# Kernel tuning notes

Measured on AMD Instinct MI355X. Metric: run time of the kernel, lower is better.

## Reference

```python
import jax, jax.numpy as jnp
import numpy as np

B, S, D, H = 2, 2048, 1024, 16
DK = D // H

def setup_inputs() -> dict:
    key = jax.random.key(0)
    ks = jax.random.split(key, 12)
    def lin(k, shape, fan_in):
        bound = 1.0 / np.sqrt(fan_in)
        return jax.random.uniform(k, shape, jnp.float32, -bound, bound)
    inp = {
        'Q': jax.random.normal(ks[0], (B, S, D), jnp.float32),
        'K': jax.random.normal(ks[1], (B, S, D), jnp.float32),
        'V': jax.random.normal(ks[2], (B, S, D), jnp.float32),
        # padding mask: last 128 key positions of batch element 0 are padding
        'padding_mask': jnp.ones((B, 1, 1, S), jnp.int32).at[0, :, :, -128:].set(0),
        # causal look-ahead mask
        'look_ahead_mask': jnp.tril(jnp.ones((S, S), jnp.int32))[None, None],
        'Wq': lin(ks[3], (D, D), D), 'bq': lin(ks[4], (D,), D),
        'Wk': lin(ks[5], (D, D), D), 'bk': lin(ks[6], (D,), D),
        'Wv': lin(ks[7], (D, D), D), 'bv': lin(ks[8], (D,), D),
        'Wo': lin(ks[9], (D, D), D), 'bo': lin(ks[10], (D,), D),
    }
    return inp

def _split_heads(x):
    # [B,S,D] -> [B,H,S,DK]
    b, s, _ = x.shape
    return x.reshape(b, s, H, DK).transpose(0, 2, 1, 3)

def reference(Q, K, V, padding_mask, look_ahead_mask, Wq, bq, Wk, bk, Wv, bv, Wo, bo):
    q = _split_heads(Q @ Wq.T + bq)  # [B,H,S,DK]
    k = _split_heads(K @ Wk.T + bk)
    v = _split_heads(V @ Wv.T + bv)
    scores = jnp.einsum('bhqd,bhkd->bhqk', q, k) / np.sqrt(DK).astype(np.float32)
    neg_inf = jnp.float32(-jnp.inf)
    scores = jnp.where(padding_mask == 0, neg_inf, scores)
    scores = jnp.where(look_ahead_mask == 0, neg_inf, scores)
    weights = jax.nn.softmax(scores, axis=-1)  # dropout is identity in eval mode
    x = jnp.einsum('bhqk,bhkd->bhqd', weights, v)  # [B,H,S,DK]
    x = x.transpose(0, 2, 1, 3).reshape(Q.shape[0], Q.shape[1], D)
    return x @ Wo.T + bo
```

## Files before the change

### kernel.cpp

```cpp
#include <hip/hip_runtime.h>
#include <hip/hip_bf16.h>

#define B_   2
#define S_   2048
#define D_   1024
#define H_   16
#define DK_  64

typedef unsigned short u16;
typedef __attribute__((ext_vector_type(8))) short bf16x8;
typedef __attribute__((ext_vector_type(4))) float f32x4;

#define CHUNK_   12
#define NSLOT_   48

static __device__ __forceinline__ u16 f2bf(float f) {
  union { float f; unsigned u; } v; v.f = f;
  unsigned r = v.u + 0x7FFF + ((v.u >> 16) & 1);
  return (u16)(r >> 16);
}

static __device__ __forceinline__ void gl_lds16(const void* g, void* l) {
  __builtin_amdgcn_global_load_lds(
      (const __attribute__((address_space(1))) void*)g,
      (__attribute__((address_space(3))) void*)l, 16, 0, 0);
}

__global__ void cvt7(const float4* __restrict__ i0, const float4* __restrict__ i1,
                     const float4* __restrict__ i2, const float4* __restrict__ i3,
                     const float4* __restrict__ i4, const float4* __restrict__ i5,
                     const float4* __restrict__ i6,
                     ushort4* __restrict__ o0, ushort4* __restrict__ o1,
                     ushort4* __restrict__ o2, ushort4* __restrict__ o3,
                     ushort4* __restrict__ o4, ushort4* __restrict__ o5,
                     ushort4* __restrict__ o6, int nbig, int nsmall) {
  int y = blockIdx.y;
  const float4* in; ushort4* out; int bound;
  switch (y) {
    case 0: in = i0; out = o0; bound = nbig; break;
    case 1: in = i1; out = o1; bound = nbig; break;
    case 2: in = i2; out = o2; bound = nbig; break;
    case 3: in = i3; out = o3; bound = nsmall; break;
    case 4: in = i4; out = o4; bound = nsmall; break;
    case 5: in = i5; out = o5; bound = nsmall; break;
    default: in = i6; out = o6; bound = nsmall; break;
  }
  int i = blockIdx.x * blockDim.x + threadIdx.x;
  if (i < bound) {
    float4 v = in[i];
    ushort4 r;
    r.x = f2bf(v.x); r.y = f2bf(v.y); r.z = f2bf(v.z); r.w = f2bf(v.w);
    out[i] = r;
  }
}

__launch_bounds__(256, 2)
__global__ void gemm_qkv(const u16* __restrict__ Xq, const u16* __restrict__ Xk, const u16* __restrict__ Xv,
                         const u16* __restrict__ Wq, const u16* __restrict__ Wk, const u16* __restrict__ Wv,
                         const float* __restrict__ bq, const float* __restrict__ bk, const float* __restrict__ bv,
                         u16* __restrict__ outq, u16* __restrict__ outk, u16* __restrict__ outv) {
  const int z = blockIdx.z;
  const u16* Am; const u16* Bm; int m0, n0;
  if (z == 2) { Am = Wv; Bm = Xv; m0 = blockIdx.x * 128; n0 = blockIdx.y * 128; }
  else if (z == 1) { Am = Xk; Bm = Wk; m0 = blockIdx.y * 128; n0 = blockIdx.x * 128; }
  else { Am = Xq; Bm = Wq; m0 = blockIdx.y * 128; n0 = blockIdx.x * 128; }
  const float* bias = (z == 0) ? bq : (z == 1) ? bk : bv;

  __shared__ __align__(16) u16 As[128 * 32];
  __shared__ __align__(16) u16 Bs[128 * 32];

  const int tid = threadIdx.x, lane = tid & 63, w = tid >> 6;
  const int q = lane >> 4, cl = lane & 15;
  const int wr = w >> 1, wc = w & 1;

  f32x4 acc[4][4] = {};

  for (int k0 = 0; k0 < D_; k0 += 32) {
#pragma unroll
    for (int i = 0; i < 2; ++i) {
      int cb = (i * 4 + w) * 64;
      int ch = cb + lane;
      int row = ch >> 2, ko = (ch & 3) << 3;
      gl_lds16(Am + (size_t)(m0 + row) * D_ + k0 + ko, As + cb * 8);
      gl_lds16(Bm + (size_t)(n0 + row) * D_ + k0 + ko, Bs + cb * 8);
    }
    __syncthreads();

    bf16x8 af[4], bfr[4];
#pragma unroll
    for (int r = 0; r < 4; ++r) af[r]  = *(const bf16x8*)(As + (wr * 64 + r * 16 + cl) * 32 + q * 8);
#pragma unroll
    for (int c = 0; c < 4; ++c) bfr[c] = *(const bf16x8*)(Bs + (wc * 64 + c * 16 + cl) * 32 + q * 8);
#pragma unroll
    for (int r = 0; r < 4; ++r)
#pragma unroll
      for (int c = 0; c < 4; ++c)
        acc[r][c] = __builtin_amdgcn_mfma_f32_16x16x32_bf16(af[r], bfr[c], acc[r][c], 0, 0, 0);
    __syncthreads();
  }

  if (z == 2) {
#pragma unroll
    for (int r = 0; r < 4; ++r) {
#pragma unroll
      for (int rr = 0; rr < 4; ++rr) {
        int j = m0 + wr * 64 + r * 16 + q * 4 + rr;
        float bval = bias[j];
        int hh = j >> 6, dk = j & 63;
#pragma unroll
        for (int c = 0; c < 4; ++c) {
          int n = n0 + wc * 64 + c * 16 + cl;
          int bb = n >> 11, s = n & (S_ - 1);
          outv[((size_t)(bb * H_ + hh) * DK_ + dk) * S_ + s] = f2bf(acc[r][c][rr] + bval);
        }
      }
    }
  } else {
    const float scale = (z == 0) ? 0.125f : 1.0f;
    u16* o = (z == 0) ? outq : outk;
#pragma unroll
    for (int c = 0; c < 4; ++c) {
      int j = n0 + wc * 64 + c * 16 + cl;
      float bval = bias[j];
      int hh = j >> 6, dk = j & 63;
#pragma unroll
      for (int r = 0; r < 4; ++r) {
#pragma unroll
        for (int rr = 0; rr < 4; ++rr) {
          int n = m0 + wr * 64 + r * 16 + q * 4 + rr;
          int bb = n >> 11, s = n & (S_ - 1);
          o[((size_t)(bb * H_ + hh) * S_ + s) * DK_ + dk] = f2bf((acc[r][c][rr] + bval) * scale);
        }
      }
    }
  }
}

__launch_bounds__(256, 4)
__global__ void attn(const u16* __restrict__ qh, const u16* __restrict__ kh,
                     const u16* __restrict__ vt, const int* __restrict__ pad,
                     u16* __restrict__ attn_out, float* __restrict__ Po, float* __restrict__ Pl) {
  __shared__ __align__(16) u16 Ks[64 * 64];
  __shared__ __align__(16) u16 Vs[64 * 64];
  __shared__ __align__(16) u16 Ps[4][16 * 72];
  __shared__ float Kbias[64];

  const int tid = threadIdx.x, lane = tid & 63, w = tid >> 6;
  const int q = lane >> 4, cl = lane & 15;
  const int h = blockIdx.y, b = blockIdx.z;

  const int x = blockIdx.x;
  int qt, ch, nch;
  if (x < 24)      { qt = 24 + x / 3;          ch = x % 3;       nch = 3; }
  else if (x < 48) { int y = x - 24; qt = 12 + y / 2; ch = y & 1; nch = 2; }
  else             { qt = x - 48;              ch = 0;           nch = 1; }
  const int qb = qt * 64;
  const int t0 = ch * CHUNK_;
  const int t1 = (qt < t0 + CHUNK_ - 1) ? qt : (t0 + CHUNK_ - 1);

  const u16* Q = qh + (size_t)(b * H_ + h) * S_ * DK_;
  const u16* K = kh + (size_t)(b * H_ + h) * S_ * DK_;
  const u16* V = vt + (size_t)(b * H_ + h) * DK_ * S_;
  const int* pm = pad + b * S_;

  const int qr0 = qb + w * 16;
  bf16x8 qf0 = *(const bf16x8*)(Q + (qr0 + cl) * DK_ + q * 8);
  bf16x8 qf1 = *(const bf16x8*)(Q + (qr0 + cl) * DK_ + 32 + q * 8);

  f32x4 o[4] = {};
  float ls[4] = {0.f, 0.f, 0.f, 0.f};
  u16* Pw = Ps[w];

  for (int it = t0; it <= t1; ++it) {
    const int kb = it << 6;
#pragma unroll
    for (int i = 0; i < 2; ++i) {
      int s = (i * 4 + w) * 64 + lane;
      int row = s >> 3;
      int c = (s & 7) ^ (row & 7);
      gl_lds16(K + (size_t)(kb + row) * DK_ + (c << 3), Ks + (size_t)s * 8);
      gl_lds16(V + (size_t)row * S_ + kb + (c << 3), Vs + (size_t)s * 8);
    }
    if (tid < 64) {
      Kbias[tid] = (pm[kb + tid] != 0) ? -6.0f : -3e38f;
    }
    __syncthreads();

    f32x4 sa[4];
#pragma unroll
    for (int ct = 0; ct < 4; ++ct) {
      int rk = ct * 16 + cl;
      int c0 = q ^ (rk & 7);
      bf16x8 kf0 = *(const bf16x8*)(Ks + rk * 64 + (c0 << 3));
      bf16x8 kf1 = *(const bf16x8*)(Ks + rk * 64 + ((c0 ^ 4) << 3));
      f32x4 zz = {};
      zz = __builtin_amdgcn_mfma_f32_16x16x32_bf16(qf0, kf0, zz, 0, 0, 0);
      zz = __builtin_amdgcn_mfma_f32_16x16x32_bf16(qf1, kf1, zz, 0, 0, 0);
      sa[ct] = zz;
    }

    if (it < qt) {
#pragma unroll
      for (int ct = 0; ct < 4; ++ct) {
        float kbv = Kbias[ct * 16 + cl];
#pragma unroll
        for (int rr = 0; rr < 4; ++rr) {
          float p = __expf(sa[ct][rr] + kbv);
          ls[rr] += p;
          Pw[(q * 4 + rr) * 72 + ct * 16 + cl] = f2bf(p);
        }
      }
    } else {
#pragma unroll
      for (int ct = 0; ct < 4; ++ct) {
        int kg = kb + ct * 16 + cl;
        float kbv = Kbias[ct * 16 + cl];
#pragma unroll
        for (int rr = 0; rr < 4; ++rr) {
          int qg = qr0 + q * 4 + rr;
          float p = (kg <= qg) ? __expf(sa[ct][rr] + kbv) : 0.f;
          ls[rr] += p;
          Pw[(q * 4 + rr) * 72 + ct * 16 + cl] = f2bf(p);
        }
      }
    }

    bf16x8 pf0 = *(const bf16x8*)(Pw + cl * 72 + q * 8);
    bf16x8 pf1 = *(const bf16x8*)(Pw + cl * 72 + 32 + q * 8);

#pragma unroll
    for (int ct = 0; ct < 4; ++ct) {
      int rv = ct * 16 + cl;
      int c0 = q ^ (rv & 7);
      bf16x8 vf0 = *(const bf16x8*)(Vs + rv * 64 + (c0 << 3));
      bf16x8 vf1 = *(const bf16x8*)(Vs + rv * 64 + ((c0 ^ 4) << 3));
      o[ct] = __builtin_amdgcn_mfma_f32_16x16x32_bf16(pf0, vf0, o[ct], 0, 0, 0);
      o[ct] = __builtin_amdgcn_mfma_f32_16x16x32_bf16(pf1, vf1, o[ct], 0, 0, 0);
    }
    __syncthreads();
  }

  if (nch == 1) {
#pragma unroll
    for (int rr = 0; rr < 4; ++rr) {
      float l = ls[rr];
      l += __shfl_xor(l, 1, 64);
      l += __shfl_xor(l, 2, 64);
      l += __shfl_xor(l, 4, 64);
      l += __shfl_xor(l, 8, 64);
      float inv = 1.0f / l;
      int qg = qr0 + q * 4 + rr;
      size_t base = (size_t)(b * S_ + qg) * D_ + h * DK_;
#pragma unroll
      for (int ct = 0; ct < 4; ++ct)
        attn_out[base + ct * 16 + cl] = f2bf(o[ct][rr] * inv);
    }
  } else {
    int pq = qt - 12;
    int off = (pq < 12) ? pq * 2 : 24 + (pq - 12) * 3;
    size_t slot = (size_t)(b * H_ + h) * NSLOT_ + off + ch;
#pragma unroll
    for (int rr = 0; rr < 4; ++rr) {
      float l = ls[rr];
      l += __shfl_xor(l, 1, 64);
      l += __shfl_xor(l, 2, 64);
      l += __shfl_xor(l, 4, 64);
      l += __shfl_xor(l, 8, 64);
      int rl = w * 16 + q * 4 + rr;
      if (cl == 0) Pl[slot * 64 + rl] = l;
      float* po = Po + ((size_t)slot * 64 + rl) * 64;
#pragma unroll
      for (int ct = 0; ct < 4; ++ct)
        po[ct * 16 + cl] = o[ct][rr];
    }
  }
}

__global__ void combine(const float* __restrict__ Po, const float* __restrict__ Pl,
                        u16* __restrict__ attn_out) {
  const int qt = 12 + blockIdx.x, h = blockIdx.y, b = blockIdx.z;
  const int nch = (qt < 24) ? 2 : 3;
  const int pq = qt - 12;
  const int off = (pq < 12) ? pq * 2 : 24 + (pq - 12) * 3;
  const size_t slot0 = (size_t)(b * H_ + h) * NSLOT_ + off;

  const int c = threadIdx.x & 63;
  const int r0 = (threadIdx.x >> 6) * 16;
#pragma unroll 4
  for (int i = 0; i < 16; ++i) {
    int r = r0 + i;
    float os = 0.f, lsum = 0.f;
    for (int ch = 0; ch < nch; ++ch) {
      os += Po[((slot0 + ch) * 64 + r) * 64 + c];
      lsum += Pl[(slot0 + ch) * 64 + r];
    }
    int qg = qt * 64 + r;
    attn_out[(size_t)(b * S_ + qg) * D_ + h * DK_ + c] = f2bf(os / lsum);
  }
}

__launch_bounds__(256, 2)
__global__ void gemm_out(const u16* __restrict__ A, const u16* __restrict__ W,
                         const float* __restrict__ bias, float* __restrict__ out) {
  __shared__ __align__(16) u16 As[128 * 32];
  __shared__ __align__(16) u16 Bs[128 * 32];

  const int tid = threadIdx.x, lane = tid & 63, w = tid >> 6;
  const int q = lane >> 4, cl = lane & 15;
  const int wr = w >> 1, wc = w & 1;
  const int m0 = blockIdx.y * 128, n0 = blockIdx.x * 128;

  f32x4 acc[4][4] = {};

  for (int k0 = 0; k0 < D_; k0 += 32) {
#pragma unroll
    for (int i = 0; i < 2; ++i) {
      int cb = (i * 4 + w) * 64;
      int ch = cb + lane;
      int row = ch >> 2, ko = (ch & 3) << 3;
      gl_lds16(A + (size_t)(m0 + row) * D_ + k0 + ko, As + cb * 8);
      gl_lds16(W + (size_t)(n0 + row) * D_ + k0 + ko, Bs + cb * 8);
    }
    __syncthreads();

    bf16x8 af[4], bfr[4];
#pragma unroll
    for (int r = 0; r < 4; ++r) af[r]  = *(const bf16x8*)(As + (wr * 64 + r * 16 + cl) * 32 + q * 8);
#pragma unroll
    for (int c = 0; c < 4; ++c) bfr[c] = *(const bf16x8*)(Bs + (wc * 64 + c * 16 + cl) * 32 + q * 8);
#pragma unroll
    for (int r = 0; r < 4; ++r)
#pragma unroll
      for (int c = 0; c < 4; ++c)
        acc[r][c] = __builtin_amdgcn_mfma_f32_16x16x32_bf16(af[r], bfr[c], acc[r][c], 0, 0, 0);
    __syncthreads();
  }

#pragma unroll
  for (int c = 0; c < 4; ++c) {
    int j = n0 + wc * 64 + c * 16 + cl;
    float bval = bias[j];
#pragma unroll
    for (int r = 0; r < 4; ++r) {
#pragma unroll
      for (int rr = 0; rr < 4; ++rr) {
        int n = m0 + wr * 64 + r * 16 + q * 4 + rr;
        out[(size_t)n * D_ + j] = acc[r][c][rr] + bval;
      }
    }
  }
}

extern "C" void kernel_launch(void* const* d_in, const int* in_sizes, int n_in,
                              void* d_out, int out_size, void* d_ws, size_t ws_size,
                              hipStream_t stream) {
  const float* Qf  = (const float*)d_in[0];
  const float* Kf  = (const float*)d_in[1];
  const float* Vf  = (const float*)d_in[2];
  const int*   pad = (const int*)d_in[3];
  const float* Wqf = (const float*)d_in[5];
  const float* bq  = (const float*)d_in[6];
  const float* Wkf = (const float*)d_in[7];
  const float* bk  = (const float*)d_in[8];
  const float* Wvf = (const float*)d_in[9];
  const float* bv  = (const float*)d_in[10];
  const float* Wof = (const float*)d_in[11];
  const float* bo  = (const float*)d_in[12];

  const size_t BSD = (size_t)B_ * S_ * D_;
  const size_t DD  = (size_t)D_ * D_;

  char* ws = (char*)d_ws;
  u16* Qb   = (u16*)ws; ws += BSD * 2;
  u16* Kb   = (u16*)ws; ws += BSD * 2;
  u16* Vb   = (u16*)ws; ws += BSD * 2;
  u16* Wqb  = (u16*)ws; ws += DD * 2;
  u16* Wkb  = (u16*)ws; ws += DD * 2;
  u16* Wvb  = (u16*)ws; ws += DD * 2;
  u16* Wob  = (u16*)ws; ws += DD * 2;
  u16* qhd  = (u16*)ws; ws += BSD * 2;
  u16* khd  = (u16*)ws; ws += BSD * 2;
  u16* vtd  = (u16*)ws; ws += BSD * 2;
  u16* attn_o = (u16*)ws; ws += BSD * 2;

  float* Po = (float*)d_ws;
  float* Pl = Po + (size_t)B_ * H_ * NSLOT_ * 64 * 64;

  const int n4 = (int)(BSD / 4);
  const int w4 = (int)(DD / 4);
  dim3 gc(n4 / 256, 7);
  cvt7<<<gc, 256, 0, stream>>>((const float4*)Qf, (const float4*)Kf, (const float4*)Vf,
                               (const float4*)Wqf, (const float4*)Wkf, (const float4*)Wvf, (const float4*)Wof,
                               (ushort4*)Qb, (ushort4*)Kb, (ushort4*)Vb,
                               (ushort4*)Wqb, (ushort4*)Wkb, (ushort4*)Wvb, (ushort4*)Wob, n4, w4);

  dim3 g1(D_ / 128, (B_ * S_) / 128, 3);
  gemm_qkv<<<g1, 256, 0, stream>>>(Qb, Kb, Vb, Wqb, Wkb, Wvb, bq, bk, bv, qhd, khd, vtd);

  dim3 g2(60, H_, B_);
  attn<<<g2, 256, 0, stream>>>(qhd, khd, vtd, pad, attn_o, Po, Pl);

  dim3 g2b(20, H_, B_);
  combine<<<g2b, 256, 0, stream>>>(Po, Pl, attn_o);

  dim3 g3(D_ / 128, (B_ * S_) / 128);
  gemm_out<<<g3, 256, 0, stream>>>(attn_o, Wob, bo, (float*)d_out);
}
```

Baseline: 257.5 us.

## Split KV range across two wave groups in-block, drop combine kernel

```diff
diff --git a/kernel.cpp b/kernel.cpp
--- a/kernel.cpp
+++ b/kernel.cpp
@@ -10,9 +10,6 @@
 typedef unsigned short u16;
 typedef __attribute__((ext_vector_type(8))) short bf16x8;
 typedef __attribute__((ext_vector_type(4))) float f32x4;
-
-#define CHUNK_   12
-#define NSLOT_   48
 
 static __device__ __forceinline__ u16 f2bf(float f) {
   union { float f; unsigned u; } v; v.f = f;
@@ -136,111 +133,140 @@
   }
 }
 
-__launch_bounds__(256, 4)
+__launch_bounds__(512, 6)
 __global__ void attn(const u16* __restrict__ qh, const u16* __restrict__ kh,
                      const u16* __restrict__ vt, const int* __restrict__ pad,
-                     u16* __restrict__ attn_out, float* __restrict__ Po, float* __restrict__ Pl) {
-  __shared__ __align__(16) u16 Ks[64 * 64];
-  __shared__ __align__(16) u16 Vs[64 * 64];
-  __shared__ __align__(16) u16 Ps[4][16 * 72];
-  __shared__ float Kbias[64];
-
-  const int tid = threadIdx.x, lane = tid & 63, w = tid >> 6;
+                     u16* __restrict__ attn_out) {
+  __shared__ __align__(16) u16 Ks[2][64 * 64];
+  __shared__ __align__(16) u16 Vs[2][64 * 64];
+  __shared__ __align__(16) u16 Ps[8][16 * 72];
+  __shared__ float Kbias[2][64];
+
+  const int tid = threadIdx.x, lane = tid & 63, wave = tid >> 6;
+  const int g = wave >> 2, gw = wave & 3, gt = tid & 255;
   const int q = lane >> 4, cl = lane & 15;
-  const int h = blockIdx.y, b = blockIdx.z;
-
-  const int x = blockIdx.x;
-  int qt, ch, nch;
-  if (x < 24)      { qt = 24 + x / 3;          ch = x % 3;       nch = 3; }
-  else if (x < 48) { int y = x - 24; qt = 12 + y / 2; ch = y & 1; nch = 2; }
-  else             { qt = x - 48;              ch = 0;           nch = 1; }
-  const int qb = qt * 64;
-  const int t0 = ch * CHUNK_;
-  const int t1 = (qt < t0 + CHUNK_ - 1) ? qt : (t0 + CHUNK_ - 1);
+  const int qt = 31 - (int)blockIdx.x;
+  const int qb = qt * 64, h = blockIdx.y, b = blockIdx.z;
+
+  const int n = qt + 1;
+  const int cnt0 = (n + 1) >> 1;
+  const int cntg = g ? (n >> 1) : cnt0;
+  const int baseg = g ? cnt0 : 0;
 
   const u16* Q = qh + (size_t)(b * H_ + h) * S_ * DK_;
   const u16* K = kh + (size_t)(b * H_ + h) * S_ * DK_;
   const u16* V = vt + (size_t)(b * H_ + h) * DK_ * S_;
   const int* pm = pad + b * S_;
 
-  const int qr0 = qb + w * 16;
+  const int qr0 = qb + gw * 16;
   bf16x8 qf0 = *(const bf16x8*)(Q + (qr0 + cl) * DK_ + q * 8);
   bf16x8 qf1 = *(const bf16x8*)(Q + (qr0 + cl) * DK_ + 32 + q * 8);
 
   f32x4 o[4] = {};
   float ls[4] = {0.f, 0.f, 0.f, 0.f};
-  u16* Pw = Ps[w];
-
-  for (int it = t0; it <= t1; ++it) {
-    const int kb = it << 6;
-#pragma unroll
-    for (int i = 0; i < 2; ++i) {
-      int s = (i * 4 + w) * 64 + lane;
-      int row = s >> 3;
-      int c = (s & 7) ^ (row & 7);
-      gl_lds16(K + (size_t)(kb + row) * DK_ + (c << 3), Ks + (size_t)s * 8);
-      gl_lds16(V + (size_t)row * S_ + kb + (c << 3), Vs + (size_t)s * 8);
-    }
-    if (tid < 64) {
-      Kbias[tid] = (pm[kb + tid] != 0) ? -6.0f : -3e38f;
-    }
-    __syncthreads();
-
-    f32x4 sa[4];
-#pragma unroll
-    for (int ct = 0; ct < 4; ++ct) {
-      int rk = ct * 16 + cl;
-      int c0 = q ^ (rk & 7);
-      bf16x8 kf0 = *(const bf16x8*)(Ks + rk * 64 + (c0 << 3));
-      bf16x8 kf1 = *(const bf16x8*)(Ks + rk * 64 + ((c0 ^ 4) << 3));
-      f32x4 zz = {};
-      zz = __builtin_amdgcn_mfma_f32_16x16x32_bf16(qf0, kf0, zz, 0, 0, 0);
-      zz = __builtin_amdgcn_mfma_f32_16x16x32_bf16(qf1, kf1, zz, 0, 0, 0);
-      sa[ct] = zz;
-    }
-
-    if (it < qt) {
+  u16* Pw = Ps[wave];
+  u16* Ksg = Ks[g];
+  u16* Vsg = Vs[g];
+
+  for (int i = 0; i < cnt0; ++i) {
+    const bool act = (i < cntg);
+    const int itg = baseg + i;
+    const int kb = itg << 6;
+
+    if (act) {
+#pragma unroll
+      for (int j = 0; j < 2; ++j) {
+        int s = (j * 4 + gw) * 64 + lane;
+        int row = s >> 3;
+        int c = (s & 7) ^ (row & 7);
+        gl_lds16(K + (size_t)(kb + row) * DK_ + (c << 3), Ksg + (size_t)s * 8);
+        gl_lds16(V + (size_t)row * S_ + kb + (c << 3), Vsg + (size_t)s * 8);
+      }
+      if (gt < 64) {
+        Kbias[g][gt] = (pm[kb + gt] != 0) ? -6.0f : -3e38f;
+      }
+    }
+    __syncthreads();
+
+    if (act) {
+      f32x4 sa[4];
 #pragma unroll
       for (int ct = 0; ct < 4; ++ct) {
-        float kbv = Kbias[ct * 16 + cl];
-#pragma unroll
-        for (int rr = 0; rr < 4; ++rr) {
-          float p = __expf(sa[ct][rr] + kbv);
-          ls[rr] += p;
-          Pw[(q * 4 + rr) * 72 + ct * 16 + cl] = f2bf(p);
+        int rk = ct * 16 + cl;
+        int c0 = q ^ (rk & 7);
+        bf16x8 kf0 = *(const bf16x8*)(Ksg + rk * 64 + (c0 << 3));
+        bf16x8 kf1 = *(const bf16x8*)(Ksg + rk * 64 + ((c0 ^ 4) << 3));
+        f32x4 zz = {};
+        zz = __builtin_amdgcn_mfma_f32_16x16x32_bf16(qf0, kf0, zz, 0, 0, 0);
+        zz = __builtin_amdgcn_mfma_f32_16x16x32_bf16(qf1, kf1, zz, 0, 0, 0);
+        sa[ct] = zz;
+      }
+
+      if (itg < qt) {
+#pragma unroll
+        for (int ct = 0; ct < 4; ++ct) {
+          float kbv = Kbias[g][ct * 16 + cl];
+#pragma unroll
+          for (int rr = 0; rr < 4; ++rr) {
+            float p = __expf(sa[ct][rr] + kbv);
+            ls[rr] += p;
+            Pw[(q * 4 + rr) * 72 + ct * 16 + cl] = f2bf(p);
+          }
         }
-      }
-    } else {
+      } else {
+#pragma unroll
+        for (int ct = 0; ct < 4; ++ct) {
+          int kg = kb + ct * 16 + cl;
+          float kbv = Kbias[g][ct * 16 + cl];
+#pragma unroll
+          for (int rr = 0; rr < 4; ++rr) {
+            int qg = qr0 + q * 4 + rr;
+            float p = (kg <= qg) ? __expf(sa[ct][rr] + kbv) : 0.f;
+            ls[rr] += p;
+            Pw[(q * 4 + rr) * 72 + ct * 16 + cl] = f2bf(p);
+          }
+        }
+      }
+
+      bf16x8 pf0 = *(const bf16x8*)(Pw + cl * 72 + q * 8);
+      bf16x8 pf1 = *(const bf16x8*)(Pw + cl * 72 + 32 + q * 8);
+
 #pragma unroll
       for (int ct = 0; ct < 4; ++ct) {
-        int kg = kb + ct * 16 + cl;
-        float kbv = Kbias[ct * 16 + cl];
-#pragma unroll
-        for (int rr = 0; rr < 4; ++rr) {
-          int qg = qr0 + q * 4 + rr;
-          float p = (kg <= qg) ? __expf(sa[ct][rr] + kbv) : 0.f;
-          ls[rr] += p;
-          Pw[(q * 4 + rr) * 72 + ct * 16 + cl] = f2bf(p);
-        }
-      }
-    }
-
-    bf16x8 pf0 = *(const bf16x8*)(Pw + cl * 72 + q * 8);
-    bf16x8 pf1 = *(const bf16x8*)(Pw + cl * 72 + 32 + q * 8);
-
-#pragma unroll
-    for (int ct = 0; ct < 4; ++ct) {
-      int rv = ct * 16 + cl;
-      int c0 = q ^ (rv & 7);
-      bf16x8 vf0 = *(const bf16x8*)(Vs + rv * 64 + (c0 << 3));
-      bf16x8 vf1 = *(const bf16x8*)(Vs + rv * 64 + ((c0 ^ 4) << 3));
-      o[ct] = __builtin_amdgcn_mfma_f32_16x16x32_bf16(pf0, vf0, o[ct], 0, 0, 0);
-      o[ct] = __builtin_amdgcn_mfma_f32_16x16x32_bf16(pf1, vf1, o[ct], 0, 0, 0);
-    }
-    __syncthreads();
-  }
-
-  if (nch == 1) {
+        int rv = ct * 16 + cl;
+        int c0 = q ^ (rv & 7);
+        bf16x8 vf0 = *(const bf16x8*)(Vsg + rv * 64 + (c0 << 3));
+        bf16x8 vf1 = *(const bf16x8*)(Vsg + rv * 64 + ((c0 ^ 4) << 3));
+        o[ct] = __builtin_amdgcn_mfma_f32_16x16x32_bf16(pf0, vf0, o[ct], 0, 0, 0);
+        o[ct] = __builtin_amdgcn_mfma_f32_16x16x32_bf16(pf1, vf1, o[ct], 0, 0, 0);
+      }
+    }
+    __syncthreads();
+  }
+
+  if (g == 1) {
+    float* So = (float*)Ps;
+    float* Sl = (float*)Ks;
+#pragma unroll
+    for (int ct = 0; ct < 4; ++ct)
+#pragma unroll
+      for (int rr = 0; rr < 4; ++rr)
+        So[gt * 17 + ct * 4 + rr] = o[ct][rr];
+#pragma unroll
+    for (int rr = 0; rr < 4; ++rr) Sl[gt * 5 + rr] = ls[rr];
+  }
+  __syncthreads();
+  if (g == 0) {
+    const float* So = (const float*)Ps;
+    const float* Sl = (const float*)Ks;
+#pragma unroll
+    for (int ct = 0; ct < 4; ++ct)
+#pragma unroll
+      for (int rr = 0; rr < 4; ++rr)
+        o[ct][rr] += So[gt * 17 + ct * 4 + rr];
+#pragma unroll
+    for (int rr = 0; rr < 4; ++rr) ls[rr] += Sl[gt * 5 + rr];
+
 #pragma unroll
     for (int rr = 0; rr < 4; ++rr) {
       float l = ls[rr];
@@ -255,47 +281,6 @@
       for (int ct = 0; ct < 4; ++ct)
         attn_out[base + ct * 16 + cl] = f2bf(o[ct][rr] * inv);
     }
-  } else {
-    int pq = qt - 12;
-    int off = (pq < 12) ? pq * 2 : 24 + (pq - 12) * 3;
-    size_t slot = (size_t)(b * H_ + h) * NSLOT_ + off + ch;
-#pragma unroll
-    for (int rr = 0; rr < 4; ++rr) {
-      float l = ls[rr];
-      l += __shfl_xor(l, 1, 64);
-      l += __shfl_xor(l, 2, 64);
-      l += __shfl_xor(l, 4, 64);
-      l += __shfl_xor(l, 8, 64);
-      int rl = w * 16 + q * 4 + rr;
-      if (cl == 0) Pl[slot * 64 + rl] = l;
-      float* po = Po + ((size_t)slot * 64 + rl) * 64;
-#pragma unroll
-      for (int ct = 0; ct < 4; ++ct)
-        po[ct * 16 + cl] = o[ct][rr];
-    }
-  }
-}
-
-__global__ void combine(const float* __restrict__ Po, const float* __restrict__ Pl,
-                        u16* __restrict__ attn_out) {
-  const int qt = 12 + blockIdx.x, h = blockIdx.y, b = blockIdx.z;
-  const int nch = (qt < 24) ? 2 : 3;
-  const int pq = qt - 12;
-  const int off = (pq < 12) ? pq * 2 : 24 + (pq - 12) * 3;
-  const size_t slot0 = (size_t)(b * H_ + h) * NSLOT_ + off;
-
-  const int c = threadIdx.x & 63;
-  const int r0 = (threadIdx.x >> 6) * 16;
-#pragma unroll 4
-  for (int i = 0; i < 16; ++i) {
-    int r = r0 + i;
-    float os = 0.f, lsum = 0.f;
-    for (int ch = 0; ch < nch; ++ch) {
-      os += Po[((slot0 + ch) * 64 + r) * 64 + c];
-      lsum += Pl[(slot0 + ch) * 64 + r];
-    }
-    int qg = qt * 64 + r;
-    attn_out[(size_t)(b * S_ + qg) * D_ + h * DK_ + c] = f2bf(os / lsum);
   }
 }
 
@@ -383,9 +368,6 @@
   u16* vtd  = (u16*)ws; ws += BSD * 2;
   u16* attn_o = (u16*)ws; ws += BSD * 2;
 
-  float* Po = (float*)d_ws;
-  float* Pl = Po + (size_t)B_ * H_ * NSLOT_ * 64 * 64;
-
   const int n4 = (int)(BSD / 4);
   const int w4 = (int)(DD / 4);
   dim3 gc(n4 / 256, 7);
@@ -397,11 +379,8 @@
   dim3 g1(D_ / 128, (B_ * S_) / 128, 3);
   gemm_qkv<<<g1, 256, 0, stream>>>(Qb, Kb, Vb, Wqb, Wkb, Wvb, bq, bk, bv, qhd, khd, vtd);
 
-  dim3 g2(60, H_, B_);
-  attn<<<g2, 256, 0, stream>>>(qhd, khd, vtd, pad, attn_o, Po, Pl);
-
-  dim3 g2b(20, H_, B_);
-  combine<<<g2b, 256, 0, stream>>>(Po, Pl, attn_o);
+  dim3 g2(32, H_, B_);
+  attn<<<g2, 512, 0, stream>>>(qhd, khd, vtd, pad, attn_o);
 
   dim3 g3(D_ / 128, (B_ * S_) / 128);
   gemm_out<<<g3, 256, 0, stream>>>(attn_o, Wob, bo, (float*)d_out);
```

New measurement: 307.2 us. 1.19x slower.

## Widen GEMM K-tile to 64 with XOR-swizzled LDS layout

Applied to the files above, without the earlier changes.

```diff
diff --git a/kernel.cpp b/kernel.cpp
--- a/kernel.cpp
+++ b/kernel.cpp
@@ -54,7 +54,7 @@
   }
 }
 
-__launch_bounds__(256, 2)
+__launch_bounds__(256, 3)
 __global__ void gemm_qkv(const u16* __restrict__ Xq, const u16* __restrict__ Xk, const u16* __restrict__ Xv,
                          const u16* __restrict__ Wq, const u16* __restrict__ Wk, const u16* __restrict__ Wv,
                          const float* __restrict__ bq, const float* __restrict__ bk, const float* __restrict__ bv,
@@ -66,8 +66,8 @@
   else { Am = Xq; Bm = Wq; m0 = blockIdx.y * 128; n0 = blockIdx.x * 128; }
   const float* bias = (z == 0) ? bq : (z == 1) ? bk : bv;
 
-  __shared__ __align__(16) u16 As[128 * 32];
-  __shared__ __align__(16) u16 Bs[128 * 32];
+  __shared__ __align__(16) u16 As[128 * 64];
+  __shared__ __align__(16) u16 Bs[128 * 64];
 
   const int tid = threadIdx.x, lane = tid & 63, w = tid >> 6;
   const int q = lane >> 4, cl = lane & 15;
@@ -75,27 +75,33 @@
 
   f32x4 acc[4][4] = {};
 
-  for (int k0 = 0; k0 < D_; k0 += 32) {
-#pragma unroll
-    for (int i = 0; i < 2; ++i) {
-      int cb = (i * 4 + w) * 64;
-      int ch = cb + lane;
-      int row = ch >> 2, ko = (ch & 3) << 3;
-      gl_lds16(Am + (size_t)(m0 + row) * D_ + k0 + ko, As + cb * 8);
-      gl_lds16(Bm + (size_t)(n0 + row) * D_ + k0 + ko, Bs + cb * 8);
-    }
-    __syncthreads();
-
-    bf16x8 af[4], bfr[4];
-#pragma unroll
-    for (int r = 0; r < 4; ++r) af[r]  = *(const bf16x8*)(As + (wr * 64 + r * 16 + cl) * 32 + q * 8);
-#pragma unroll
-    for (int c = 0; c < 4; ++c) bfr[c] = *(const bf16x8*)(Bs + (wc * 64 + c * 16 + cl) * 32 + q * 8);
-#pragma unroll
-    for (int r = 0; r < 4; ++r)
+  for (int k0 = 0; k0 < D_; k0 += 64) {
+#pragma unroll
+    for (int i = 0; i < 4; ++i) {
+      int ch = i * 256 + tid;
+      int row = ch >> 3, c = ch & 7;
+      int gc = (c ^ (row & 7)) << 3;
+      gl_lds16(Am + (size_t)(m0 + row) * D_ + k0 + gc, As + ch * 8);
+      gl_lds16(Bm + (size_t)(n0 + row) * D_ + k0 + gc, Bs + ch * 8);
+    }
+    __syncthreads();
+
+#pragma unroll
+    for (int kk = 0; kk < 2; ++kk) {
+      bf16x8 af[4], bfr[4];
+      int jc = (kk << 2) | q;
+#pragma unroll
+      for (int r = 0; r < 4; ++r)
+        af[r]  = *(const bf16x8*)(As + (wr * 64 + r * 16 + cl) * 64 + ((jc ^ (cl & 7)) << 3));
 #pragma unroll
       for (int c = 0; c < 4; ++c)
-        acc[r][c] = __builtin_amdgcn_mfma_f32_16x16x32_bf16(af[r], bfr[c], acc[r][c], 0, 0, 0);
+        bfr[c] = *(const bf16x8*)(Bs + (wc * 64 + c * 16 + cl) * 64 + ((jc ^ (cl & 7)) << 3));
+#pragma unroll
+      for (int r = 0; r < 4; ++r)
+#pragma unroll
+        for (int c = 0; c < 4; ++c)
+          acc[r][c] = __builtin_amdgcn_mfma_f32_16x16x32_bf16(af[r], bfr[c], acc[r][c], 0, 0, 0);
+    }
     __syncthreads();
   }
 
@@ -299,11 +305,11 @@
   }
 }
 
-__launch_bounds__(256, 2)
+__launch_bounds__(256, 3)
 __global__ void gemm_out(const u16* __restrict__ A, const u16* __restrict__ W,
                          const float* __restrict__ bias, float* __restrict__ out) {
-  __shared__ __align__(16) u16 As[128 * 32];
-  __shared__ __align__(16) u16 Bs[128 * 32];
+  __shared__ __align__(16) u16 As[128 * 64];
+  __shared__ __align__(16) u16 Bs[128 * 64];
 
   const int tid = threadIdx.x, lane = tid & 63, w = tid >> 6;
   const int q = lane >> 4, cl = lane & 15;
@@ -312,27 +318,33 @@
 
   f32x4 acc[4][4] = {};
 
-  for (int k0 = 0; k0 < D_; k0 += 32) {
-#pragma unroll
-    for (int i = 0; i < 2; ++i) {
-      int cb = (i * 4 + w) * 64;
-      int ch = cb + lane;
-      int row = ch >> 2, ko = (ch & 3) << 3;
-      gl_lds16(A + (size_t)(m0 + row) * D_ + k0 + ko, As + cb * 8);
-      gl_lds16(W + (size_t)(n0 + row) * D_ + k0 + ko, Bs + cb * 8);
-    }
-    __syncthreads();
-
-    bf16x8 af[4], bfr[4];
-#pragma unroll
-    for (int r = 0; r < 4; ++r) af[r]  = *(const bf16x8*)(As + (wr * 64 + r * 16 + cl) * 32 + q * 8);
-#pragma unroll
-    for (int c = 0; c < 4; ++c) bfr[c] = *(const bf16x8*)(Bs + (wc * 64 + c * 16 + cl) * 32 + q * 8);
-#pragma unroll
-    for (int r = 0; r < 4; ++r)
+  for (int k0 = 0; k0 < D_; k0 += 64) {
+#pragma unroll
+    for (int i = 0; i < 4; ++i) {
+      int ch = i * 256 + tid;
+      int row = ch >> 3, c = ch & 7;
+      int gc = (c ^ (row & 7)) << 3;
+      gl_lds16(A + (size_t)(m0 + row) * D_ + k0 + gc, As + ch * 8);
+      gl_lds16(W + (size_t)(n0 + row) * D_ + k0 + gc, Bs + ch * 8);
+    }
+    __syncthreads();
+
+#pragma unroll
+    for (int kk = 0; kk < 2; ++kk) {
+      bf16x8 af[4], bfr[4];
+      int jc = (kk << 2) | q;
+#pragma unroll
+      for (int r = 0; r < 4; ++r)
+        af[r]  = *(const bf16x8*)(As + (wr * 64 + r * 16 + cl) * 64 + ((jc ^ (cl & 7)) << 3));
 #pragma unroll
       for (int c = 0; c < 4; ++c)
-        acc[r][c] = __builtin_amdgcn_mfma_f32_16x16x32_bf16(af[r], bfr[c], acc[r][c], 0, 0, 0);
+        bfr[c] = *(const bf16x8*)(Bs + (wc * 64 + c * 16 + cl) * 64 + ((jc ^ (cl & 7)) << 3));
+#pragma unroll
+      for (int r = 0; r < 4; ++r)
+#pragma unroll
+        for (int c = 0; c < 4; ++c)
+          acc[r][c] = __builtin_amdgcn_mfma_f32_16x16x32_bf16(af[r], bfr[c], acc[r][c], 0, 0, 0);
+    }
     __syncthreads();
   }
 
```

New measurement: 255.9 us. Within noise of the previous version (-0.6%).

## Double-buffer LDS in QKV and output GEMMs, shrink out tile, flatten combine

Applied to the files above, without the earlier changes.

```diff
diff --git a/kernel.cpp b/kernel.cpp
--- a/kernel.cpp
+++ b/kernel.cpp
@@ -54,7 +54,7 @@
   }
 }
 
-__launch_bounds__(256, 2)
+__launch_bounds__(256, 3)
 __global__ void gemm_qkv(const u16* __restrict__ Xq, const u16* __restrict__ Xk, const u16* __restrict__ Xv,
                          const u16* __restrict__ Wq, const u16* __restrict__ Wk, const u16* __restrict__ Wv,
                          const float* __restrict__ bq, const float* __restrict__ bk, const float* __restrict__ bv,
@@ -66,8 +66,8 @@
   else { Am = Xq; Bm = Wq; m0 = blockIdx.y * 128; n0 = blockIdx.x * 128; }
   const float* bias = (z == 0) ? bq : (z == 1) ? bk : bv;
 
-  __shared__ __align__(16) u16 As[128 * 32];
-  __shared__ __align__(16) u16 Bs[128 * 32];
+  __shared__ __align__(16) u16 As[2][128 * 32];
+  __shared__ __align__(16) u16 Bs[2][128 * 32];
 
   const int tid = threadIdx.x, lane = tid & 63, w = tid >> 6;
   const int q = lane >> 4, cl = lane & 15;
@@ -75,28 +75,44 @@
 
   f32x4 acc[4][4] = {};
 
+#pragma unroll
+  for (int i = 0; i < 2; ++i) {
+    int cb = (i * 4 + w) * 64;
+    int ch = cb + lane;
+    int row = ch >> 2, ko = (ch & 3) << 3;
+    gl_lds16(Am + (size_t)(m0 + row) * D_ + ko, As[0] + cb * 8);
+    gl_lds16(Bm + (size_t)(n0 + row) * D_ + ko, Bs[0] + cb * 8);
+  }
+  __syncthreads();
+
+  int cur = 0;
   for (int k0 = 0; k0 < D_; k0 += 32) {
-#pragma unroll
-    for (int i = 0; i < 2; ++i) {
-      int cb = (i * 4 + w) * 64;
-      int ch = cb + lane;
-      int row = ch >> 2, ko = (ch & 3) << 3;
-      gl_lds16(Am + (size_t)(m0 + row) * D_ + k0 + ko, As + cb * 8);
-      gl_lds16(Bm + (size_t)(n0 + row) * D_ + k0 + ko, Bs + cb * 8);
-    }
-    __syncthreads();
-
+    if (k0 + 32 < D_) {
+#pragma unroll
+      for (int i = 0; i < 2; ++i) {
+        int cb = (i * 4 + w) * 64;
+        int ch = cb + lane;
+        int row = ch >> 2, ko = (ch & 3) << 3;
+        gl_lds16(Am + (size_t)(m0 + row) * D_ + k0 + 32 + ko, As[cur ^ 1] + cb * 8);
+        gl_lds16(Bm + (size_t)(n0 + row) * D_ + k0 + 32 + ko, Bs[cur ^ 1] + cb * 8);
+      }
+    }
+
+    const u16* Ac = As[cur];
+    const u16* Bc = Bs[cur];
     bf16x8 af[4], bfr[4];
 #pragma unroll
-    for (int r = 0; r < 4; ++r) af[r]  = *(const bf16x8*)(As + (wr * 64 + r * 16 + cl) * 32 + q * 8);
-#pragma unroll
-    for (int c = 0; c < 4; ++c) bfr[c] = *(const bf16x8*)(Bs + (wc * 64 + c * 16 + cl) * 32 + q * 8);
+    for (int r = 0; r < 4; ++r) af[r]  = *(const bf16x8*)(Ac + (wr * 64 + r * 16 + cl) * 32 + q * 8);
+#pragma unroll
+    for (int c = 0; c < 4; ++c) bfr[c] = *(const bf16x8*)(Bc + (wc * 64 + c * 16 + cl) * 32 + q * 8);
 #pragma unroll
     for (int r = 0; r < 4; ++r)
 #pragma unroll
       for (int c = 0; c < 4; ++c)
         acc[r][c] = __builtin_amdgcn_mfma_f32_16x16x32_bf16(af[r], bfr[c], acc[r][c], 0, 0, 0);
+
     __syncthreads();
+    cur ^= 1;
   }
 
   if (z == 2) {
@@ -278,62 +294,84 @@
 
 __global__ void combine(const float* __restrict__ Po, const float* __restrict__ Pl,
                         u16* __restrict__ attn_out) {
-  const int qt = 12 + blockIdx.x, h = blockIdx.y, b = blockIdx.z;
+  const int x = blockIdx.x, h = blockIdx.y, b = blockIdx.z;
+  const int qt = 12 + (x >> 4);
+  const int inner = ((x & 15) << 8) + threadIdx.x;
+  const int r = inner >> 6, c = inner & 63;
+
   const int nch = (qt < 24) ? 2 : 3;
   const int pq = qt - 12;
   const int off = (pq < 12) ? pq * 2 : 24 + (pq - 12) * 3;
   const size_t slot0 = (size_t)(b * H_ + h) * NSLOT_ + off;
 
-  const int c = threadIdx.x & 63;
-  const int r0 = (threadIdx.x >> 6) * 16;
-#pragma unroll 4
-  for (int i = 0; i < 16; ++i) {
-    int r = r0 + i;
-    float os = 0.f, lsum = 0.f;
-    for (int ch = 0; ch < nch; ++ch) {
-      os += Po[((slot0 + ch) * 64 + r) * 64 + c];
-      lsum += Pl[(slot0 + ch) * 64 + r];
-    }
-    int qg = qt * 64 + r;
-    attn_out[(size_t)(b * S_ + qg) * D_ + h * DK_ + c] = f2bf(os / lsum);
-  }
+  float os = 0.f, lsum = 0.f;
+  for (int ch = 0; ch < nch; ++ch) {
+    os += Po[((slot0 + ch) * 64 + r) * 64 + c];
+    lsum += Pl[(slot0 + ch) * 64 + r];
+  }
+  int qg = qt * 64 + r;
+  attn_out[(size_t)(b * S_ + qg) * D_ + h * DK_ + c] = f2bf(os / lsum);
 }
 
 __launch_bounds__(256, 2)
 __global__ void gemm_out(const u16* __restrict__ A, const u16* __restrict__ W,
                          const float* __restrict__ bias, float* __restrict__ out) {
-  __shared__ __align__(16) u16 As[128 * 32];
-  __shared__ __align__(16) u16 Bs[128 * 32];
+  __shared__ __align__(16) u16 As[2][64 * 32];
+  __shared__ __align__(16) u16 Bs[2][128 * 32];
 
   const int tid = threadIdx.x, lane = tid & 63, w = tid >> 6;
   const int q = lane >> 4, cl = lane & 15;
   const int wr = w >> 1, wc = w & 1;
-  const int m0 = blockIdx.y * 128, n0 = blockIdx.x * 128;
-
-  f32x4 acc[4][4] = {};
-
+  const int m0 = blockIdx.y * 64, n0 = blockIdx.x * 128;
+
+  f32x4 acc[2][4] = {};
+
+  {
+    int cb = w * 64;
+    int chA = cb + lane;
+    int rowA = chA >> 2, koA = (chA & 3) << 3;
+    gl_lds16(A + (size_t)(m0 + rowA) * D_ + koA, As[0] + cb * 8);
+#pragma unroll
+    for (int i = 0; i < 2; ++i) {
+      int cbB = (i * 4 + w) * 64;
+      int chB = cbB + lane;
+      int rowB = chB >> 2, koB = (chB & 3) << 3;
+      gl_lds16(W + (size_t)(n0 + rowB) * D_ + koB, Bs[0] + cbB * 8);
+    }
+  }
+  __syncthreads();
+
+  int cur = 0;
   for (int k0 = 0; k0 < D_; k0 += 32) {
-#pragma unroll
-    for (int i = 0; i < 2; ++i) {
-      int cb = (i * 4 + w) * 64;
-      int ch = cb + lane;
-      int row = ch >> 2, ko = (ch & 3) << 3;
-      gl_lds16(A + (size_t)(m0 + row) * D_ + k0 + ko, As + cb * 8);
-      gl_lds16(W + (size_t)(n0 + row) * D_ + k0 + ko, Bs + cb * 8);
-    }
-    __syncthreads();
-
-    bf16x8 af[4], bfr[4];
-#pragma unroll
-    for (int r = 0; r < 4; ++r) af[r]  = *(const bf16x8*)(As + (wr * 64 + r * 16 + cl) * 32 + q * 8);
-#pragma unroll
-    for (int c = 0; c < 4; ++c) bfr[c] = *(const bf16x8*)(Bs + (wc * 64 + c * 16 + cl) * 32 + q * 8);
-#pragma unroll
-    for (int r = 0; r < 4; ++r)
+    if (k0 + 32 < D_) {
+      int cb = w * 64;
+      int chA = cb + lane;
+      int rowA = chA >> 2, koA = (chA & 3) << 3;
+      gl_lds16(A + (size_t)(m0 + rowA) * D_ + k0 + 32 + koA, As[cur ^ 1] + cb * 8);
+#pragma unroll
+      for (int i = 0; i < 2; ++i) {
+        int cbB = (i * 4 + w) * 64;
+        int chB = cbB + lane;
+        int rowB = chB >> 2, koB = (chB & 3) << 3;
+        gl_lds16(W + (size_t)(n0 + rowB) * D_ + k0 + 32 + koB, Bs[cur ^ 1] + cbB * 8);
+      }
+    }
+
+    const u16* Ac = As[cur];
+    const u16* Bc = Bs[cur];
+    bf16x8 af[2], bfr[4];
+#pragma unroll
+    for (int r = 0; r < 2; ++r) af[r]  = *(const bf16x8*)(Ac + (wr * 32 + r * 16 + cl) * 32 + q * 8);
+#pragma unroll
+    for (int c = 0; c < 4; ++c) bfr[c] = *(const bf16x8*)(Bc + (wc * 64 + c * 16 + cl) * 32 + q * 8);
+#pragma unroll
+    for (int r = 0; r < 2; ++r)
 #pragma unroll
       for (int c = 0; c < 4; ++c)
         acc[r][c] = __builtin_amdgcn_mfma_f32_16x16x32_bf16(af[r], bfr[c], acc[r][c], 0, 0, 0);
+
     __syncthreads();
+    cur ^= 1;
   }
 
 #pragma unroll
@@ -341,10 +379,10 @@
     int j = n0 + wc * 64 + c * 16 + cl;
     float bval = bias[j];
 #pragma unroll
-    for (int r = 0; r < 4; ++r) {
+    for (int r = 0; r < 2; ++r) {
 #pragma unroll
       for (int rr = 0; rr < 4; ++rr) {
-        int n = m0 + wr * 64 + r * 16 + q * 4 + rr;
+        int n = m0 + wr * 32 + r * 16 + q * 4 + rr;
         out[(size_t)n * D_ + j] = acc[r][c][rr] + bval;
       }
     }
@@ -400,9 +438,9 @@
   dim3 g2(60, H_, B_);
   attn<<<g2, 256, 0, stream>>>(qhd, khd, vtd, pad, attn_o, Po, Pl);
 
-  dim3 g2b(20, H_, B_);
+  dim3 g2b(320, H_, B_);
   combine<<<g2b, 256, 0, stream>>>(Po, Pl, attn_o);
 
-  dim3 g3(D_ / 128, (B_ * S_) / 128);
+  dim3 g3(D_ / 128, (B_ * S_) / 64);
   gemm_out<<<g3, 256, 0, stream>>>(attn_o, Wob, bo, (float*)d_out);
 }
```

Result: faster. 250.9 us (-2.6%).
